# Kernel optimization log

Measured on AMD Instinct MI355X. Metric: run time of the kernel, lower is better.

## Reference

```python
import jax, jax.numpy as jnp
import numpy as np

V, D, B, NEG = 100000, 128, 4096, 5
D_INNER = int(D * 2.0 * 2 / 3)  # nGPT FF inner dim = 170

def l2norm(t, axis=-1):
    return t / jnp.linalg.norm(t, axis=axis, keepdims=True)

def setup_inputs() -> dict:
    key = jax.random.key(0)
    ks = jax.random.split(key, 8)
    return {
        "input_ids": jax.random.randint(ks[0], (B,), 0, V),
        "target_ids": jax.random.randint(ks[1], (B,), 0, V),
        "neg_ids": jax.random.randint(ks[2], (B, NEG), 0, V),
        "W_in": jax.random.normal(ks[3], (V, D), jnp.float32) * (1.0 / np.sqrt(D)),
        "W_out": jax.random.normal(ks[4], (V, D), jnp.float32) * (1.0 / np.sqrt(D)),
        "W_hidden": jax.random.normal(ks[5], (D_INNER, D), jnp.float32) * 0.02,
        "W_gate": jax.random.normal(ks[6], (D_INNER, D), jnp.float32) * 0.02,
        "W_ff_out": jax.random.normal(ks[7], (D, D_INNER), jnp.float32) * 0.02,
        "hidden_scale": jnp.ones((D_INNER,), jnp.float32),
        "gate_scale": jnp.ones((D_INNER,), jnp.float32),
        "logit_scale": jnp.full((V,), D ** -0.5, dtype=jnp.float32),  # Scale param init = s_logit_scale
    }

def reference(input_ids, target_ids, neg_ids, W_in, W_out, W_hidden, W_gate,
              W_ff_out, hidden_scale, gate_scale, logit_scale):
    # skipgram: gather normalized input embeddings
    emb = l2norm(W_in)[input_ids]                                  # (B, D)
    # nGPT FeedForward: silu-gated, weights l2-normalized on input dim
    h = (emb @ l2norm(W_hidden).T) * hidden_scale                  # (B, D_INNER)
    g = (emb @ l2norm(W_gate).T) * gate_scale * jnp.sqrt(jnp.float32(D))
    x = jax.nn.silu(g) * h
    x = x @ l2norm(W_ff_out, axis=0).T                             # (B, D), to_out norm_dim_in=False
    # logits over full vocab, scaled by Scale(): param * (init/scale)
    scale_eff = logit_scale * (1.0 / (D ** -0.5))                  # (V,)
    logits = (x @ l2norm(W_out).T) * scale_eff                     # (B, V)
    # negative-sampling loss: gather positive + sampled negative logits
    pos = jnp.take_along_axis(logits, target_ids[:, None], axis=1)  # (B, 1)
    neg = jnp.take_along_axis(logits, neg_ids, axis=1)              # (B, NEG)
    positive_loss = jax.nn.log_sigmoid(pos).mean()
    negative_loss = jax.nn.log_sigmoid(-neg).mean()
    return -(positive_loss + negative_loss)
```

## Files before the change

kernel.cpp:

```cpp
#include <hip/hip_runtime.h>
#include <math.h>

#define DD   128
#define DI   170
#define BB   4096
#define NNEG 5
#define ROWS 4
#define NBLK (BB / ROWS)
#define SQRT_D 11.3137084989847603904f

__device__ __forceinline__ float wave_bcast_sum(float v) {
#pragma unroll
    for (int m = 1; m < 64; m <<= 1) v += __shfl_xor(v, m, 64);
    return v;
}

__global__ __launch_bounds__(256) void norms_kernel(
    const float* __restrict__ W_hidden,
    const float* __restrict__ W_gate,
    const float* __restrict__ W_ff_out,
    float* __restrict__ inv_h,
    float* __restrict__ inv_g,
    float* __restrict__ inv_f,
    float* __restrict__ out)
{
    if (blockIdx.x == 0 && threadIdx.x == 0) out[0] = 0.0f;
    const int wave = threadIdx.x >> 6;
    const int lane = threadIdx.x & 63;
    const int v = blockIdx.x * 4 + wave;
    if (v >= 3 * DI) return;
    float s;
    if (v < 2 * DI) {
        const float* W = (v < DI) ? W_hidden : W_gate;
        const int row = (v < DI) ? v : v - DI;
        float2 p = ((const float2*)(W + (long)row * DD))[lane];
        s = p.x * p.x + p.y * p.y;
    } else {
        const int c = v - 2 * DI;
        float a = W_ff_out[(long)(2 * lane)     * DI + c];
        float b = W_ff_out[(long)(2 * lane + 1) * DI + c];
        s = a * a + b * b;
    }
    s = wave_bcast_sum(s);
    if (lane == 0) {
        float inv = rsqrtf(s);
        if (v < DI)            inv_h[v] = inv;
        else if (v < 2 * DI)   inv_g[v - DI] = inv;
        else                   inv_f[v - 2 * DI] = inv;
    }
}

__global__ __launch_bounds__(256) void main_kernel(
    const int*   __restrict__ input_ids,
    const int*   __restrict__ target_ids,
    const int*   __restrict__ neg_ids,
    const float* __restrict__ W_in,
    const float* __restrict__ W_out,
    const float* __restrict__ W_hidden,
    const float* __restrict__ W_gate,
    const float* __restrict__ W_ff_out,
    const float* __restrict__ hidden_scale,
    const float* __restrict__ gate_scale,
    const float* __restrict__ logit_scale,
    const float* __restrict__ inv_h,
    const float* __restrict__ inv_g,
    const float* __restrict__ inv_f,
    float* __restrict__ out)
{
    __shared__ float s_emb[ROWS][DD];
    __shared__ float s_x[ROWS][DI + 2];
    __shared__ float s_xout[ROWS][DD];
    __shared__ float s_red[4];

    const int tid  = threadIdx.x;
    const int wave = tid >> 6;
    const int lane = tid & 63;
    const int b0   = blockIdx.x * ROWS;

#pragma unroll
    for (int k = 0; k < ROWS / 4; ++k) {
        const int r  = wave + 4 * k;
        const int id = input_ids[b0 + r];
        float2 p = ((const float2*)(W_in + (long)id * DD))[lane];
        float s  = wave_bcast_sum(p.x * p.x + p.y * p.y);
        float inv = rsqrtf(s);
        s_emb[r][2 * lane]     = p.x * inv;
        s_emb[r][2 * lane + 1] = p.y * inv;
    }
    __syncthreads();

    if (tid < DI) {
        const int i = tid;
        float ah[ROWS], ag[ROWS];
#pragma unroll
        for (int r = 0; r < ROWS; ++r) { ah[r] = 0.0f; ag[r] = 0.0f; }
        const float4* wh = (const float4*)(W_hidden + (long)i * DD);
        const float4* wg = (const float4*)(W_gate   + (long)i * DD);
        for (int d4 = 0; d4 < DD / 4; ++d4) {
            float4 h4 = wh[d4];
            float4 g4 = wg[d4];
#pragma unroll
            for (int r = 0; r < ROWS; ++r) {
                float4 e4 = ((const float4*)s_emb[r])[d4];
                ah[r] += e4.x * h4.x + e4.y * h4.y + e4.z * h4.z + e4.w * h4.w;
                ag[r] += e4.x * g4.x + e4.y * g4.y + e4.z * g4.z + e4.w * g4.w;
            }
        }
        const float hs = hidden_scale[i] * inv_h[i];
        const float gs = gate_scale[i]   * inv_g[i] * SQRT_D;
        const float fi = inv_f[i];
#pragma unroll
        for (int r = 0; r < ROWS; ++r) {
            float h = ah[r] * hs;
            float g = ag[r] * gs;
            float x = (g / (1.0f + __expf(-g))) * h;
            s_x[r][i] = x * fi;
        }
    }
    __syncthreads();

    {
        const int dd = tid & 127;
        const int r0 = tid >> 7;
        float acc[ROWS / 2];
#pragma unroll
        for (int k = 0; k < ROWS / 2; ++k) acc[k] = 0.0f;
        const float2* wrow = (const float2*)(W_ff_out + (long)dd * DI);
        for (int i2 = 0; i2 < DI / 2; ++i2) {
            float2 wf = wrow[i2];
#pragma unroll
            for (int k = 0; k < ROWS / 2; ++k) {
                const int r = r0 + 2 * k;
                float2 xv = *(const float2*)&s_x[r][2 * i2];
                acc[k] += xv.x * wf.x + xv.y * wf.y;
            }
        }
#pragma unroll
        for (int k = 0; k < ROWS / 2; ++k) s_xout[r0 + 2 * k][dd] = acc[k];
    }
    __syncthreads();

    float wacc = 0.0f;
    for (int t = wave; t < ROWS * (1 + NNEG); t += 4) {
        const int r  = t / (1 + NNEG);
        const int jj = t % (1 + NNEG);
        const int bidx = b0 + r;
        const int id = (jj == 0) ? target_ids[bidx] : neg_ids[bidx * NNEG + jj - 1];
        const float* wrow = W_out + (long)id * DD;
        float w0 = wrow[lane], w1 = wrow[64 + lane];
        float x0 = s_xout[r][lane], x1 = s_xout[r][64 + lane];
        float dot = w0 * x0 + w1 * x1;
        float ss  = w0 * w0 + w1 * w1;
#pragma unroll
        for (int m = 1; m < 64; m <<= 1) {
            dot += __shfl_xor(dot, m, 64);
            ss  += __shfl_xor(ss,  m, 64);
        }
        const float logit = dot * rsqrtf(ss) * logit_scale[id] * SQRT_D;
        const float z  = (jj == 0) ? logit : -logit;
        const float ls = fminf(z, 0.0f) - log1pf(__expf(-fabsf(z)));
        wacc += (jj == 0) ? ls * (1.0f / BB) : ls * (1.0f / (BB * NNEG));
    }
    if (lane == 0) s_red[wave] = wacc;
    __syncthreads();
    if (tid == 0) {
        float tot = s_red[0] + s_red[1] + s_red[2] + s_red[3];
        atomicAdd(out, -tot);
    }
}

extern "C" void kernel_launch(void* const* d_in, const int* in_sizes, int n_in,
                              void* d_out, int out_size, void* d_ws, size_t ws_size,
                              hipStream_t stream) {
    (void)in_sizes; (void)n_in; (void)out_size; (void)ws_size;
    const int*   input_ids    = (const int*)  d_in[0];
    const int*   target_ids   = (const int*)  d_in[1];
    const int*   neg_ids      = (const int*)  d_in[2];
    const float* W_in         = (const float*)d_in[3];
    const float* W_out        = (const float*)d_in[4];
    const float* W_hidden     = (const float*)d_in[5];
    const float* W_gate       = (const float*)d_in[6];
    const float* W_ff_out     = (const float*)d_in[7];
    const float* hidden_scale = (const float*)d_in[8];
    const float* gate_scale   = (const float*)d_in[9];
    const float* logit_scale  = (const float*)d_in[10];
    float* out   = (float*)d_out;
    float* inv_h = (float*)d_ws;
    float* inv_g = inv_h + DI;
    float* inv_f = inv_g + DI;

    norms_kernel<<<128, 256, 0, stream>>>(W_hidden, W_gate, W_ff_out,
                                          inv_h, inv_g, inv_f, out);
    main_kernel<<<NBLK, 256, 0, stream>>>(input_ids, target_ids, neg_ids,
                                          W_in, W_out, W_hidden, W_gate, W_ff_out,
                                          hidden_scale, gate_scale, logit_scale,
                                          inv_h, inv_g, inv_f, out);
}
```

Before: 174.5 us.

## Stage FF weights through swizzled shared memory and double rows per block

Doubles the rows per block to 8 and stages W_hidden/W_gate in 32-column slabs, then W_ff_out in 64-row slabs, through shared memory. XOR and rotation swizzles avoid LDS bank conflicts, and the loads become coalesced instead of per-thread strided row reads. The goal is to cut redundant global and L2 weight traffic per batch row and to fix the uncoalesced W_ff_out access. The cost is more barriers, more LDS use (around 45KB), and half as many blocks.

```diff
diff --git a/kernel.cpp b/kernel.cpp
--- a/kernel.cpp
+++ b/kernel.cpp
@@ -1,12 +1,14 @@
 #include <hip/hip_runtime.h>
 #include <math.h>
 
-#define DD   128
-#define DI   170
-#define BB   4096
-#define NNEG 5
-#define ROWS 4
-#define NBLK (BB / ROWS)
+#define DD    128
+#define DI    170
+#define DIP   176
+#define NC44  44
+#define BB    4096
+#define NNEG  5
+#define ROWS  8
+#define NBLK  (BB / ROWS)
 #define SQRT_D 11.3137084989847603904f
 
 __device__ __forceinline__ float wave_bcast_sum(float v) {
@@ -67,15 +69,22 @@
     const float* __restrict__ inv_f,
     float* __restrict__ out)
 {
-    __shared__ float s_emb[ROWS][DD];
-    __shared__ float s_x[ROWS][DI + 2];
-    __shared__ float s_xout[ROWS][DD];
+    union SharedU {
+        struct { float wh[DI][32]; float wg[DI][32]; } p2;
+        float wf[64][DIP];
+    };
+    __shared__ __align__(16) SharedU u;
+    __shared__ __align__(16) float s_emb[ROWS][DD];
+    __shared__ __align__(16) float s_x[ROWS][DIP];
+    __shared__ __align__(16) float s_xout[ROWS][DD];
     __shared__ float s_red[4];
 
     const int tid  = threadIdx.x;
     const int wave = tid >> 6;
     const int lane = tid & 63;
     const int b0   = blockIdx.x * ROWS;
+    const int srow = lane >> 3;
+    const int schk = lane & 7;
 
 #pragma unroll
     for (int k = 0; k < ROWS / 4; ++k) {
@@ -87,58 +96,100 @@
         s_emb[r][2 * lane]     = p.x * inv;
         s_emb[r][2 * lane + 1] = p.y * inv;
     }
-    __syncthreads();
+
+    float ah[ROWS], ag[ROWS];
+#pragma unroll
+    for (int r = 0; r < ROWS; ++r) { ah[r] = 0.0f; ag[r] = 0.0f; }
+
+    for (int slab = 0; slab < 4; ++slab) {
+        const long dofs = slab * 32 + schk * 4;
+#pragma unroll
+        for (int rnd = 0; rnd < 6; ++rnd) {
+            const int i = rnd * 32 + wave * 8 + srow;
+            if (i < DI) {
+                const int pc = schk ^ (i & 7);
+                float4 v = *(const float4*)(W_hidden + (long)i * DD + dofs);
+                *(float4*)&u.p2.wh[i][pc * 4] = v;
+                v = *(const float4*)(W_gate + (long)i * DD + dofs);
+                *(float4*)&u.p2.wg[i][pc * 4] = v;
+            }
+        }
+        __syncthreads();
+        if (tid < DI) {
+            const int sw = tid & 7;
+            const float4* whr = (const float4*)&u.p2.wh[tid][0];
+            const float4* wgr = (const float4*)&u.p2.wg[tid][0];
+#pragma unroll
+            for (int c = 0; c < 8; ++c) {
+                const int pc = c ^ sw;
+                float4 h4 = whr[pc];
+                float4 g4 = wgr[pc];
+                const int dc = slab * 8 + c;
+#pragma unroll
+                for (int r = 0; r < ROWS; ++r) {
+                    float4 e4 = ((const float4*)s_emb[r])[dc];
+                    ah[r] += e4.x * h4.x + e4.y * h4.y + e4.z * h4.z + e4.w * h4.w;
+                    ag[r] += e4.x * g4.x + e4.y * g4.y + e4.z * g4.z + e4.w * g4.w;
+                }
+            }
+        }
+        __syncthreads();
+    }
 
     if (tid < DI) {
-        const int i = tid;
-        float ah[ROWS], ag[ROWS];
-#pragma unroll
-        for (int r = 0; r < ROWS; ++r) { ah[r] = 0.0f; ag[r] = 0.0f; }
-        const float4* wh = (const float4*)(W_hidden + (long)i * DD);
-        const float4* wg = (const float4*)(W_gate   + (long)i * DD);
-        for (int d4 = 0; d4 < DD / 4; ++d4) {
-            float4 h4 = wh[d4];
-            float4 g4 = wg[d4];
-#pragma unroll
-            for (int r = 0; r < ROWS; ++r) {
-                float4 e4 = ((const float4*)s_emb[r])[d4];
-                ah[r] += e4.x * h4.x + e4.y * h4.y + e4.z * h4.z + e4.w * h4.w;
-                ag[r] += e4.x * g4.x + e4.y * g4.y + e4.z * g4.z + e4.w * g4.w;
-            }
-        }
-        const float hs = hidden_scale[i] * inv_h[i];
-        const float gs = gate_scale[i]   * inv_g[i] * SQRT_D;
-        const float fi = inv_f[i];
+        const float hs = hidden_scale[tid] * inv_h[tid];
+        const float gs = gate_scale[tid]   * inv_g[tid] * SQRT_D;
+        const float fi = inv_f[tid];
 #pragma unroll
         for (int r = 0; r < ROWS; ++r) {
             float h = ah[r] * hs;
             float g = ag[r] * gs;
             float x = (g / (1.0f + __expf(-g))) * h;
-            s_x[r][i] = x * fi;
-        }
-    }
-    __syncthreads();
-
-    {
-        const int dd = tid & 127;
-        const int r0 = tid >> 7;
-        float acc[ROWS / 2];
-#pragma unroll
-        for (int k = 0; k < ROWS / 2; ++k) acc[k] = 0.0f;
-        const float2* wrow = (const float2*)(W_ff_out + (long)dd * DI);
-        for (int i2 = 0; i2 < DI / 2; ++i2) {
-            float2 wf = wrow[i2];
-#pragma unroll
-            for (int k = 0; k < ROWS / 2; ++k) {
-                const int r = r0 + 2 * k;
-                float2 xv = *(const float2*)&s_x[r][2 * i2];
-                acc[k] += xv.x * wf.x + xv.y * wf.y;
-            }
-        }
-#pragma unroll
-        for (int k = 0; k < ROWS / 2; ++k) s_xout[r0 + 2 * k][dd] = acc[k];
-    }
-    __syncthreads();
+            s_x[r][tid] = x * fi;
+        }
+    } else if (tid < DIP) {
+#pragma unroll
+        for (int r = 0; r < ROWS; ++r) s_x[r][tid] = 0.0f;
+    }
+
+    const int r0 = wave;
+    for (int slab = 0; slab < 2; ++slab) {
+#pragma unroll
+        for (int rr = 0; rr < 2; ++rr) {
+            const int dlr = rr * 32 + wave * 8 + srow;
+            const float* gsrc = W_ff_out + (long)(slab * 64 + dlr) * DI;
+            for (int jr = 0; jr < 11; ++jr) {
+                const int j = jr * 8 + schk;
+                float2 v = make_float2(0.0f, 0.0f);
+                if (j < 85) v = *(const float2*)(gsrc + 2 * j);
+                const int c  = j >> 1;
+                int pc = c + dlr;
+                pc %= NC44;
+                *(float2*)&u.wf[dlr][pc * 4 + (j & 1) * 2] = v;
+            }
+        }
+        __syncthreads();
+        {
+            const int dl = lane;
+            float acc0 = 0.0f, acc1 = 0.0f;
+            const float4* wfr = (const float4*)&u.wf[dl][0];
+            const float4* x0r = (const float4*)&s_x[r0][0];
+            const float4* x1r = (const float4*)&s_x[r0 + 4][0];
+            int pc = (dl >= NC44) ? dl - NC44 : dl;
+            for (int c = 0; c < NC44; ++c) {
+                float4 w4 = wfr[pc];
+                float4 xa = x0r[c];
+                float4 xb = x1r[c];
+                acc0 += w4.x * xa.x + w4.y * xa.y + w4.z * xa.z + w4.w * xa.w;
+                acc1 += w4.x * xb.x + w4.y * xb.y + w4.z * xb.z + w4.w * xb.w;
+                ++pc; if (pc == NC44) pc = 0;
+            }
+            const int dd = slab * 64 + dl;
+            s_xout[r0][dd]     = acc0;
+            s_xout[r0 + 4][dd] = acc1;
+        }
+        __syncthreads();
+    }
 
     float wacc = 0.0f;
     for (int t = wave; t < ROWS * (1 + NNEG); t += 4) {
```

Result: slower. 187.8 us (+7.6%).

## Pre-transpose and pre-scale FF weights, interleave as float4, double rows per block

Applied to the files above, without the earlier changes.

The prep kernel now folds the l2 norms and the hidden/gate/ff_out scales into transposed, float4-interleaved, zero-padded copies of W_hidden, W_gate and W_ff_out in the workspace. Consecutive threads in the main kernel then read consecutive float4 weights, so loads coalesce instead of striding by a full row. ROWS goes from 4 to 8, which doubles reuse of each weight load and halves the block count. The cost is a larger prep pass, more registers per thread, and fewer blocks to hide latency.

```diff
diff --git a/kernel.cpp b/kernel.cpp
--- a/kernel.cpp
+++ b/kernel.cpp
@@ -1,13 +1,20 @@
 #include <hip/hip_runtime.h>
 #include <math.h>
 
-#define DD   128
-#define DI   170
-#define BB   4096
-#define NNEG 5
-#define ROWS 4
-#define NBLK (BB / ROWS)
+#define DD    128
+#define DI    170
+#define DIP   176
+#define ND4   32
+#define NI4   43
+#define BB    4096
+#define NNEG  5
+#define ROWS  8
+#define NBLK  (BB / ROWS)
 #define SQRT_D 11.3137084989847603904f
+
+#define WS_WHT 0
+#define WS_WGT (ND4 * DIP * 4)
+#define WS_WFT (2 * ND4 * DIP * 4)
 
 __device__ __forceinline__ float wave_bcast_sum(float v) {
 #pragma unroll
@@ -15,38 +22,63 @@
     return v;
 }
 
-__global__ __launch_bounds__(256) void norms_kernel(
+__global__ __launch_bounds__(256) void prep_kernel(
     const float* __restrict__ W_hidden,
     const float* __restrict__ W_gate,
     const float* __restrict__ W_ff_out,
-    float* __restrict__ inv_h,
-    float* __restrict__ inv_g,
-    float* __restrict__ inv_f,
+    const float* __restrict__ hidden_scale,
+    const float* __restrict__ gate_scale,
+    float* __restrict__ ws,
     float* __restrict__ out)
 {
     if (blockIdx.x == 0 && threadIdx.x == 0) out[0] = 0.0f;
     const int wave = threadIdx.x >> 6;
     const int lane = threadIdx.x & 63;
-    const int v = blockIdx.x * 4 + wave;
-    if (v >= 3 * DI) return;
-    float s;
-    if (v < 2 * DI) {
-        const float* W = (v < DI) ? W_hidden : W_gate;
-        const int row = (v < DI) ? v : v - DI;
-        float2 p = ((const float2*)(W + (long)row * DD))[lane];
-        s = p.x * p.x + p.y * p.y;
-    } else {
-        const int c = v - 2 * DI;
-        float a = W_ff_out[(long)(2 * lane)     * DI + c];
-        float b = W_ff_out[(long)(2 * lane + 1) * DI + c];
-        s = a * a + b * b;
-    }
-    s = wave_bcast_sum(s);
-    if (lane == 0) {
-        float inv = rsqrtf(s);
-        if (v < DI)            inv_h[v] = inv;
-        else if (v < 2 * DI)   inv_g[v - DI] = inv;
-        else                   inv_f[v - 2 * DI] = inv;
+    const int t = blockIdx.x * 4 + wave;
+    float* whT = ws + WS_WHT;
+    float* wgT = ws + WS_WGT;
+    float* wfT = ws + WS_WFT;
+
+    if (t < DI) {
+        const int v = t;
+        float a = W_ff_out[(long)(2 * lane)     * DI + v];
+        float b = W_ff_out[(long)(2 * lane + 1) * DI + v];
+        float cf = wave_bcast_sum(a * a + b * b);
+        float2 ph = ((const float2*)(W_hidden + (long)v * DD))[lane];
+        float2 pg = ((const float2*)(W_gate   + (long)v * DD))[lane];
+        float sh = wave_bcast_sum(ph.x * ph.x + ph.y * ph.y);
+        float sg = wave_bcast_sum(pg.x * pg.x + pg.y * pg.y);
+        const float whs = rsqrtf(sh) * hidden_scale[v] * rsqrtf(cf);
+        const float wgs = rsqrtf(sg) * gate_scale[v] * SQRT_D;
+        const int d4   = lane >> 1;
+        const int half = lane & 1;
+        float2* dh = (float2*)(whT + ((long)d4 * DIP + v) * 4 + half * 2);
+        *dh = make_float2(ph.x * whs, ph.y * whs);
+        float2* dg = (float2*)(wgT + ((long)d4 * DIP + v) * 4 + half * 2);
+        *dg = make_float2(pg.x * wgs, pg.y * wgs);
+    } else if (t < DI + NI4) {
+        const int i4 = t - DI;
+#pragma unroll
+        for (int rr = 0; rr < 2; ++rr) {
+            const int dd = rr * 64 + lane;
+            float4 v4;
+            if (i4 < 42) {
+                float2 lo = *(const float2*)(W_ff_out + (long)dd * DI + 4 * i4);
+                float2 hi = *(const float2*)(W_ff_out + (long)dd * DI + 4 * i4 + 2);
+                v4 = make_float4(lo.x, lo.y, hi.x, hi.y);
+            } else {
+                float2 lo = *(const float2*)(W_ff_out + (long)dd * DI + 168);
+                v4 = make_float4(lo.x, lo.y, 0.0f, 0.0f);
+            }
+            *(float4*)(wfT + ((long)i4 * DD + dd) * 4) = v4;
+        }
+    } else if (t == DI + NI4 || t == DI + NI4 + 1) {
+        float* base = (t == DI + NI4) ? whT : wgT;
+        for (int idx = lane; idx < ND4 * 6; idx += 64) {
+            const int d4 = idx / 6, c = idx % 6;
+            *(float4*)(base + ((long)d4 * DIP + DI + c) * 4) =
+                make_float4(0.0f, 0.0f, 0.0f, 0.0f);
+        }
     }
 }
 
@@ -56,26 +88,23 @@
     const int*   __restrict__ neg_ids,
     const float* __restrict__ W_in,
     const float* __restrict__ W_out,
-    const float* __restrict__ W_hidden,
-    const float* __restrict__ W_gate,
-    const float* __restrict__ W_ff_out,
-    const float* __restrict__ hidden_scale,
-    const float* __restrict__ gate_scale,
     const float* __restrict__ logit_scale,
-    const float* __restrict__ inv_h,
-    const float* __restrict__ inv_g,
-    const float* __restrict__ inv_f,
+    const float* __restrict__ ws,
     float* __restrict__ out)
 {
-    __shared__ float s_emb[ROWS][DD];
-    __shared__ float s_x[ROWS][DI + 2];
-    __shared__ float s_xout[ROWS][DD];
+    __shared__ __align__(16) float s_emb[ROWS][DD];
+    __shared__ __align__(16) float s_x[ROWS][DIP];
+    __shared__ __align__(16) float s_xout[ROWS][DD];
     __shared__ float s_red[4];
 
     const int tid  = threadIdx.x;
     const int wave = tid >> 6;
     const int lane = tid & 63;
     const int b0   = blockIdx.x * ROWS;
+
+    const float4* whT4 = (const float4*)(ws + WS_WHT);
+    const float4* wgT4 = (const float4*)(ws + WS_WGT);
+    const float4* wfT4 = (const float4*)(ws + WS_WFT);
 
 #pragma unroll
     for (int k = 0; k < ROWS / 4; ++k) {
@@ -89,16 +118,14 @@
     }
     __syncthreads();
 
-    if (tid < DI) {
+    if (tid < DIP) {
         const int i = tid;
         float ah[ROWS], ag[ROWS];
 #pragma unroll
         for (int r = 0; r < ROWS; ++r) { ah[r] = 0.0f; ag[r] = 0.0f; }
-        const float4* wh = (const float4*)(W_hidden + (long)i * DD);
-        const float4* wg = (const float4*)(W_gate   + (long)i * DD);
-        for (int d4 = 0; d4 < DD / 4; ++d4) {
-            float4 h4 = wh[d4];
-            float4 g4 = wg[d4];
+        for (int d4 = 0; d4 < ND4; ++d4) {
+            float4 h4 = whT4[d4 * DIP + i];
+            float4 g4 = wgT4[d4 * DIP + i];
 #pragma unroll
             for (int r = 0; r < ROWS; ++r) {
                 float4 e4 = ((const float4*)s_emb[r])[d4];
@@ -106,15 +133,12 @@
                 ag[r] += e4.x * g4.x + e4.y * g4.y + e4.z * g4.z + e4.w * g4.w;
             }
         }
-        const float hs = hidden_scale[i] * inv_h[i];
-        const float gs = gate_scale[i]   * inv_g[i] * SQRT_D;
-        const float fi = inv_f[i];
 #pragma unroll
         for (int r = 0; r < ROWS; ++r) {
-            float h = ah[r] * hs;
-            float g = ag[r] * gs;
+            float h = ah[r];
+            float g = ag[r];
             float x = (g / (1.0f + __expf(-g))) * h;
-            s_x[r][i] = x * fi;
+            s_x[r][i] = x;
         }
     }
     __syncthreads();
@@ -122,21 +146,20 @@
     {
         const int dd = tid & 127;
         const int r0 = tid >> 7;
-        float acc[ROWS / 2];
-#pragma unroll
-        for (int k = 0; k < ROWS / 2; ++k) acc[k] = 0.0f;
-        const float2* wrow = (const float2*)(W_ff_out + (long)dd * DI);
-        for (int i2 = 0; i2 < DI / 2; ++i2) {
-            float2 wf = wrow[i2];
-#pragma unroll
-            for (int k = 0; k < ROWS / 2; ++k) {
+        float acc[4];
+#pragma unroll
+        for (int k = 0; k < 4; ++k) acc[k] = 0.0f;
+        for (int i4 = 0; i4 < NI4; ++i4) {
+            float4 w4 = wfT4[i4 * DD + dd];
+#pragma unroll
+            for (int k = 0; k < 4; ++k) {
                 const int r = r0 + 2 * k;
-                float2 xv = *(const float2*)&s_x[r][2 * i2];
-                acc[k] += xv.x * wf.x + xv.y * wf.y;
+                float4 x4 = ((const float4*)s_x[r])[i4];
+                acc[k] += w4.x * x4.x + w4.y * x4.y + w4.z * x4.z + w4.w * x4.w;
             }
         }
 #pragma unroll
-        for (int k = 0; k < ROWS / 2; ++k) s_xout[r0 + 2 * k][dd] = acc[k];
+        for (int k = 0; k < 4; ++k) s_xout[r0 + 2 * k][dd] = acc[k];
     }
     __syncthreads();
 
@@ -184,15 +207,11 @@
     const float* hidden_scale = (const float*)d_in[8];
     const float* gate_scale   = (const float*)d_in[9];
     const float* logit_scale  = (const float*)d_in[10];
-    float* out   = (float*)d_out;
-    float* inv_h = (float*)d_ws;
-    float* inv_g = inv_h + DI;
-    float* inv_f = inv_g + DI;
-
-    norms_kernel<<<128, 256, 0, stream>>>(W_hidden, W_gate, W_ff_out,
-                                          inv_h, inv_g, inv_f, out);
+    float* out = (float*)d_out;
+    float* ws  = (float*)d_ws;
+
+    prep_kernel<<<54, 256, 0, stream>>>(W_hidden, W_gate, W_ff_out,
+                                        hidden_scale, gate_scale, ws, out);
     main_kernel<<<NBLK, 256, 0, stream>>>(input_ids, target_ids, neg_ids,
-                                          W_in, W_out, W_hidden, W_gate, W_ff_out,
-                                          hidden_scale, gate_scale, logit_scale,
-                                          inv_h, inv_g, inv_f, out);
-}
+                                          W_in, W_out, logit_scale, ws, out);
+}
```

Measured after the change: 166.5 us. 4.6% less time.
